# Performance work log

Measured on AMD Instinct MI355X. Metric: run time of the kernel, lower is better.

The kernel has to match this reference:

```python
import jax, jax.numpy as jnp
import numpy as np

B, N_NODES, N_ELEM, N_GP, N_EN = 4, 1_000_000, 500_000, 9, 8


def setup_inputs() -> dict:
    key = jax.random.key(0)
    k1, k2, k3 = jax.random.split(key, 3)
    inputs = jax.random.normal(k1, (B, N_NODES, 2), dtype=jnp.float32)
    # shape-function spatial derivatives per element / gauss point: [nE, nGP, 8, 2]
    shpdx = jax.random.normal(k2, (N_ELEM, N_GP, N_EN, 2), dtype=jnp.float32)
    # 0-based element connectivity (original code stores 1-based and subtracts 1)
    elem_nodes = jax.random.randint(k3, (N_ELEM, N_EN), 0, N_NODES, dtype=jnp.int32)
    return {"inputs": inputs, "shpdx": shpdx, "elem_nodes": elem_nodes}


def reference(inputs, shpdx, elem_nodes):
    # gather nodal displacements per element: [b, nE, 8, 2]
    disp = jnp.take(inputs, elem_nodes, axis=1)
    # displacement gradient at each gauss point:
    # dd[b,e,g,n,l] = sum_k shpdx[e,g,k,l] * disp[b,e,k,n]  -> [b, nE, nGP, 2, 2]
    dd = jnp.einsum('egkl,bekn->begnl', shpdx, disp)
    e_xx = dd[..., 0, 0]
    e_yy = dd[..., 1, 1]
    e_xy = 0.5 * (dd[..., 0, 1] + dd[..., 1, 0])
    e = jnp.stack([e_xx, e_yy, e_xy], axis=-1)  # [b, nE, nGP, 3]
    return e.reshape(e.shape[0], -1, 3)  # [b, nE*nGP, 3]
```

## Files before the change

### kernel.cpp

```cpp
#include <hip/hip_runtime.h>

constexpr int B       = 4;
constexpr int N_NODES = 1000000;
constexpr int N_ELEM  = 500000;
constexpr int N_GP    = 9;
constexpr int N_EN    = 8;

__device__ __forceinline__ unsigned f2bf(float f) {
    unsigned u = __builtin_bit_cast(unsigned, f);
    unsigned r = u + 0x7fffu + ((u >> 16) & 1u);
    return r >> 16;
}
__device__ __forceinline__ float bflo(unsigned w) {
    return __builtin_bit_cast(float, w << 16);
}
__device__ __forceinline__ float bfhi(unsigned w) {
    return __builtin_bit_cast(float, w & 0xffff0000u);
}

__global__ __launch_bounds__(256) void transpose_nodes_bf16(
    const float* __restrict__ inputs,
    uint4*       __restrict__ tn)
{
    int n = blockIdx.x * blockDim.x + threadIdx.x;
    if (n >= N_NODES) return;
    const float2* in2 = reinterpret_cast<const float2*>(inputs);
    float2 a0 = in2[(size_t)0 * N_NODES + n];
    float2 a1 = in2[(size_t)1 * N_NODES + n];
    float2 a2 = in2[(size_t)2 * N_NODES + n];
    float2 a3 = in2[(size_t)3 * N_NODES + n];
    uint4 w;
    w.x = f2bf(a0.x) | (f2bf(a0.y) << 16);
    w.y = f2bf(a1.x) | (f2bf(a1.y) << 16);
    w.z = f2bf(a2.x) | (f2bf(a2.y) << 16);
    w.w = f2bf(a3.x) | (f2bf(a3.y) << 16);
    tn[n] = w;
}

__global__ __launch_bounds__(256, 6) void kinematic_bf16(
    const uint4* __restrict__ tn,
    const float* __restrict__ shpdx,
    const int*   __restrict__ elem,
    float*       __restrict__ out)
{
    const int total = N_ELEM * N_GP;
    int tid = blockIdx.x * blockDim.x + threadIdx.x;
    if (tid >= total) return;

    int e = tid / N_GP;

    const int4* ep = reinterpret_cast<const int4*>(elem + (size_t)e * N_EN);
    int4 n0 = ep[0];
    int4 n1 = ep[1];
    int nd[8] = { n0.x, n0.y, n0.z, n0.w, n1.x, n1.y, n1.z, n1.w };

    uint4 g[8];
    #pragma unroll
    for (int k = 0; k < 8; ++k) g[k] = tn[nd[k]];

    const float4* sp = reinterpret_cast<const float4*>(shpdx) + (size_t)tid * 4;
    float4 s0 = sp[0];
    float4 s1 = sp[1];
    float4 s2 = sp[2];
    float4 s3 = sp[3];
    float sx[8] = { s0.x, s0.z, s1.x, s1.z, s2.x, s2.z, s3.x, s3.z };
    float sy[8] = { s0.y, s0.w, s1.y, s1.w, s2.y, s2.w, s3.y, s3.w };

    float axx[B] = {0.f, 0.f, 0.f, 0.f};
    float ayy[B] = {0.f, 0.f, 0.f, 0.f};
    float axy[B] = {0.f, 0.f, 0.f, 0.f};

    #pragma unroll
    for (int k = 0; k < 8; ++k) {
        unsigned w0 = g[k].x, w1 = g[k].y, w2 = g[k].z, w3 = g[k].w;
        float dx[B] = { bflo(w0), bflo(w1), bflo(w2), bflo(w3) };
        float dy[B] = { bfhi(w0), bfhi(w1), bfhi(w2), bfhi(w3) };
        #pragma unroll
        for (int b = 0; b < B; ++b) {
            axx[b] = fmaf(sx[k], dx[b], axx[b]);
            ayy[b] = fmaf(sy[k], dy[b], ayy[b]);
            axy[b] = fmaf(sy[k], dx[b], fmaf(sx[k], dy[b], axy[b]));
        }
    }

    #pragma unroll
    for (int b = 0; b < B; ++b) {
        size_t o = ((size_t)b * total + (size_t)tid) * 3;
        out[o + 0] = axx[b];
        out[o + 1] = ayy[b];
        out[o + 2] = 0.5f * axy[b];
    }
}

__global__ __launch_bounds__(256) void kinematic_kernel(
    const float* __restrict__ inputs,
    const float* __restrict__ shpdx,
    const int*   __restrict__ elem,
    float*       __restrict__ out)
{
    const int total = N_ELEM * N_GP;
    int tid = blockIdx.x * blockDim.x + threadIdx.x;
    if (tid >= total) return;

    int e = tid / N_GP;

    const float4* sp = reinterpret_cast<const float4*>(shpdx) + (size_t)tid * 4;
    float4 s0 = sp[0];
    float4 s1 = sp[1];
    float4 s2 = sp[2];
    float4 s3 = sp[3];
    float sx[8] = { s0.x, s0.z, s1.x, s1.z, s2.x, s2.z, s3.x, s3.z };
    float sy[8] = { s0.y, s0.w, s1.y, s1.w, s2.y, s2.w, s3.y, s3.w };

    const int4* ep = reinterpret_cast<const int4*>(elem + (size_t)e * N_EN);
    int4 n0 = ep[0];
    int4 n1 = ep[1];
    int nd[8] = { n0.x, n0.y, n0.z, n0.w, n1.x, n1.y, n1.z, n1.w };

    #pragma unroll
    for (int b = 0; b < B; ++b) {
        const float2* inb = reinterpret_cast<const float2*>(inputs) + (size_t)b * N_NODES;
        float2 d[8];
        #pragma unroll
        for (int k = 0; k < 8; ++k) d[k] = inb[nd[k]];

        float axx = 0.f, ayy = 0.f, axy = 0.f;
        #pragma unroll
        for (int k = 0; k < 8; ++k) {
            axx = fmaf(sx[k], d[k].x, axx);
            ayy = fmaf(sy[k], d[k].y, ayy);
            axy = fmaf(sy[k], d[k].x, fmaf(sx[k], d[k].y, axy));
        }

        size_t o = ((size_t)b * total + (size_t)tid) * 3;
        out[o + 0] = axx;
        out[o + 1] = ayy;
        out[o + 2] = 0.5f * axy;
    }
}

extern "C" void kernel_launch(void* const* d_in, const int* in_sizes, int n_in,
                              void* d_out, int out_size, void* d_ws, size_t ws_size,
                              hipStream_t stream) {
    const float* inputs = (const float*)d_in[0];
    const float* shpdx  = (const float*)d_in[1];
    const int*   elem   = (const int*)d_in[2];
    float* out = (float*)d_out;

    const int total = N_ELEM * N_GP;
    const int block = 256;
    const int grid  = (total + block - 1) / block;

    const size_t tn_bytes = (size_t)N_NODES * sizeof(uint4);

    if (ws_size >= tn_bytes) {
        uint4* tn = (uint4*)d_ws;
        transpose_nodes_bf16<<<(N_NODES + block - 1) / block, block, 0, stream>>>(inputs, tn);
        kinematic_bf16<<<grid, block, 0, stream>>>(tn, shpdx, elem, out);
    } else {
        kinematic_kernel<<<grid, block, 0, stream>>>(inputs, shpdx, elem, out);
    }
}
```

Baseline: 197.6 us.

## Gather element nodes once per element into LDS and stage coalesced vector output stores

Each block now handles 28 elements. One thread per element-node gathers the packed bf16 node row into shared memory, so each node is fetched once instead of once per Gauss point (nine times). Results are staged in LDS and written out as coalesced 16-byte nontemporal stores, and shpdx is read with nontemporal loads. The cost is two block barriers, only 252 of 256 threads doing work, and more LDS per block, which may limit occupancy.

```diff
diff --git a/kernel.cpp b/kernel.cpp
--- a/kernel.cpp
+++ b/kernel.cpp
@@ -5,6 +5,12 @@
 constexpr int N_ELEM  = 500000;
 constexpr int N_GP    = 9;
 constexpr int N_EN    = 8;
+
+constexpr int EPB     = 28;
+constexpr int TOTALGP = N_ELEM * N_GP;
+constexpr int OUTQ4   = TOTALGP * 3 / 4;
+
+using f32x4 = __attribute__((ext_vector_type(4))) float;
 
 __device__ __forceinline__ unsigned f2bf(float f) {
     unsigned u = __builtin_bit_cast(unsigned, f);
@@ -37,58 +43,83 @@
     tn[n] = w;
 }
 
-__global__ __launch_bounds__(256, 6) void kinematic_bf16(
+__global__ __launch_bounds__(256, 8) void kinematic_lds(
     const uint4* __restrict__ tn,
     const float* __restrict__ shpdx,
     const int*   __restrict__ elem,
     float*       __restrict__ out)
 {
-    const int total = N_ELEM * N_GP;
-    int tid = blockIdx.x * blockDim.x + threadIdx.x;
-    if (tid >= total) return;
+    __shared__ uint4 gbuf[EPB * 9];
+    __shared__ float obuf[B * EPB * 27];
 
-    int e = tid / N_GP;
+    const int l  = threadIdx.x;
+    const int e0 = blockIdx.x * EPB;
+    const int nel = (N_ELEM - e0 < EPB) ? (N_ELEM - e0) : EPB;
 
-    const int4* ep = reinterpret_cast<const int4*>(elem + (size_t)e * N_EN);
-    int4 n0 = ep[0];
-    int4 n1 = ep[1];
-    int nd[8] = { n0.x, n0.y, n0.z, n0.w, n1.x, n1.y, n1.z, n1.w };
+    if (l < nel * N_EN) {
+        const int el = l >> 3;
+        const int k  = l & 7;
+        const int nd = elem[(e0 + el) * N_EN + k];
+        gbuf[el * 9 + k] = tn[nd];
+    }
 
-    uint4 g[8];
-    #pragma unroll
-    for (int k = 0; k < 8; ++k) g[k] = tn[nd[k]];
+    const bool active = l < nel * N_GP;
+    f32x4 s0 = {}, s1 = {}, s2 = {}, s3 = {};
+    if (active) {
+        const f32x4* sp = reinterpret_cast<const f32x4*>(shpdx)
+                        + ((size_t)e0 * N_GP + l) * 4;
+        s0 = __builtin_nontemporal_load(sp + 0);
+        s1 = __builtin_nontemporal_load(sp + 1);
+        s2 = __builtin_nontemporal_load(sp + 2);
+        s3 = __builtin_nontemporal_load(sp + 3);
+    }
 
-    const float4* sp = reinterpret_cast<const float4*>(shpdx) + (size_t)tid * 4;
-    float4 s0 = sp[0];
-    float4 s1 = sp[1];
-    float4 s2 = sp[2];
-    float4 s3 = sp[3];
-    float sx[8] = { s0.x, s0.z, s1.x, s1.z, s2.x, s2.z, s3.x, s3.z };
-    float sy[8] = { s0.y, s0.w, s1.y, s1.w, s2.y, s2.w, s3.y, s3.w };
+    __syncthreads();
 
-    float axx[B] = {0.f, 0.f, 0.f, 0.f};
-    float ayy[B] = {0.f, 0.f, 0.f, 0.f};
-    float axy[B] = {0.f, 0.f, 0.f, 0.f};
+    if (active) {
+        const int el = l / N_GP;
+        const float sx[8] = { s0[0], s0[2], s1[0], s1[2], s2[0], s2[2], s3[0], s3[2] };
+        const float sy[8] = { s0[1], s0[3], s1[1], s1[3], s2[1], s2[3], s3[1], s3[3] };
 
-    #pragma unroll
-    for (int k = 0; k < 8; ++k) {
-        unsigned w0 = g[k].x, w1 = g[k].y, w2 = g[k].z, w3 = g[k].w;
-        float dx[B] = { bflo(w0), bflo(w1), bflo(w2), bflo(w3) };
-        float dy[B] = { bfhi(w0), bfhi(w1), bfhi(w2), bfhi(w3) };
+        float axx[B] = {0.f, 0.f, 0.f, 0.f};
+        float ayy[B] = {0.f, 0.f, 0.f, 0.f};
+        float axy[B] = {0.f, 0.f, 0.f, 0.f};
+
+        #pragma unroll
+        for (int k = 0; k < 8; ++k) {
+            uint4 g = gbuf[el * 9 + k];
+            unsigned w0 = g.x, w1 = g.y, w2 = g.z, w3 = g.w;
+            float dx[B] = { bflo(w0), bflo(w1), bflo(w2), bflo(w3) };
+            float dy[B] = { bfhi(w0), bfhi(w1), bfhi(w2), bfhi(w3) };
+            #pragma unroll
+            for (int b = 0; b < B; ++b) {
+                axx[b] = fmaf(sx[k], dx[b], axx[b]);
+                ayy[b] = fmaf(sy[k], dy[b], ayy[b]);
+                axy[b] = fmaf(sy[k], dx[b], fmaf(sx[k], dy[b], axy[b]));
+            }
+        }
+
         #pragma unroll
         for (int b = 0; b < B; ++b) {
-            axx[b] = fmaf(sx[k], dx[b], axx[b]);
-            ayy[b] = fmaf(sy[k], dy[b], ayy[b]);
-            axy[b] = fmaf(sy[k], dx[b], fmaf(sx[k], dy[b], axy[b]));
+            obuf[b * (EPB * 27) + l * 3 + 0] = axx[b];
+            obuf[b * (EPB * 27) + l * 3 + 1] = ayy[b];
+            obuf[b * (EPB * 27) + l * 3 + 2] = 0.5f * axy[b];
         }
     }
 
+    __syncthreads();
+
+    const int q4 = (27 * nel) >> 2;
+    const f32x4* ob4  = reinterpret_cast<const f32x4*>(obuf);
+    f32x4*       out4 = reinterpret_cast<f32x4*>(out);
+    const size_t base4 = (size_t)blockIdx.x * (EPB * 27 / 4);
+
     #pragma unroll
     for (int b = 0; b < B; ++b) {
-        size_t o = ((size_t)b * total + (size_t)tid) * 3;
-        out[o + 0] = axx[b];
-        out[o + 1] = ayy[b];
-        out[o + 2] = 0.5f * axy[b];
+        for (int w = l; w < q4; w += 256) {
+            __builtin_nontemporal_store(ob4[b * (EPB * 27 / 4) + w],
+                                        &out4[(size_t)b * OUTQ4 + base4 + w]);
+        }
     }
 }
 
@@ -147,17 +178,17 @@
     const int*   elem   = (const int*)d_in[2];
     float* out = (float*)d_out;
 
-    const int total = N_ELEM * N_GP;
     const int block = 256;
-    const int grid  = (total + block - 1) / block;
-
     const size_t tn_bytes = (size_t)N_NODES * sizeof(uint4);
 
     if (ws_size >= tn_bytes) {
         uint4* tn = (uint4*)d_ws;
         transpose_nodes_bf16<<<(N_NODES + block - 1) / block, block, 0, stream>>>(inputs, tn);
-        kinematic_bf16<<<grid, block, 0, stream>>>(tn, shpdx, elem, out);
+        const int grid = (N_ELEM + EPB - 1) / EPB;
+        kinematic_lds<<<grid, block, 0, stream>>>(tn, shpdx, elem, out);
     } else {
+        const int total = N_ELEM * N_GP;
+        const int grid  = (total + block - 1) / block;
         kinematic_kernel<<<grid, block, 0, stream>>>(inputs, shpdx, elem, out);
     }
 }
```

Result: slower. 293.8 us (+48.7%).
